# Optimization experiments

Hardware: AMD Instinct MI355X
Metric: run time of the kernel (lower is better)

Reference implementation:

```python
import jax, jax.numpy as jnp
import numpy as np

B, T, D, F, E, K = 2, 2048, 1024, 4096, 8, 2

def setup_inputs() -> dict:
    key = jax.random.key(0)
    k0, k1, k2, k3 = jax.random.split(key, 4)
    return {
        "x": jax.random.normal(k0, (B, T, D), jnp.float32),
        "Wg": jax.random.normal(k1, (D, E), jnp.float32) * (D ** -0.5),
        "W1": jax.random.normal(k2, (E, D, F), jnp.float32) * (D ** -0.5),
        "b1": jnp.zeros((E, F), jnp.float32),
        "W2": jax.random.normal(k3, (E, F, D), jnp.float32) * (F ** -0.5),
        "b2": jnp.zeros((E, D), jnp.float32),
        "topk": K,
    }

def reference(x, Wg, W1, b1, W2, b2, topk):
    n_experts = Wg.shape[-1]
    # Gating logits [B, T, E]
    gating = jnp.einsum('btd,de->bte', x, Wg)
    _, idx = jax.lax.top_k(gating, topk)
    # 0/1 mask of selected experts per token [B, T, E]
    mask = jax.nn.one_hot(idx, n_experts, dtype=x.dtype).sum(axis=-2)
    # Source does `gating -= 1/mask - 1`: no-op where mask==1, -inf where mask==0
    gate = jax.nn.softmax(jnp.where(mask > 0, gating, -jnp.inf), axis=-1)
    # Dense masked per-expert compute, exactly as the source (expert(x * mask_e))
    xm = x[:, :, None, :] * mask[:, :, :, None]          # [B, T, E, D]
    h = jax.nn.gelu(jnp.einsum('bted,edf->btef', xm, W1) + b1)  # [B, T, E, F]
    out_e = jnp.einsum('btef,efd->bted', h, W2) + b2     # [B, T, E, D]
    # Gate and sum over experts
    return jnp.sum(out_e * gate[..., None], axis=-2)      # [B, T, D]
```

## Files before the change

### kernel.cpp

```cpp
#include <hip/hip_runtime.h>
#include <hip/hip_bf16.h>
#include <math.h>

#define NB 2
#define NT 2048
#define NTOK 4096
#define DD 1024
#define FF 4096
#define NE 8
#define KSEL 2
#define BM 128
#define BN 128
#define BK 64
#define ROWCAP 9216
#define ROWTILES 72
#define KP2 2

typedef __attribute__((ext_vector_type(8))) short short8_t;
typedef __attribute__((ext_vector_type(4))) float f32x4;

__device__ __forceinline__ unsigned short f2bf(float f){
  unsigned u = __float_as_uint(f);
  unsigned r = (u + 0x7fffu + ((u >> 16) & 1u)) >> 16;
  return (unsigned short)r;
}

__device__ __forceinline__ int xcd_swz(int lin, int nwg){
  int q = nwg >> 3, r = nwg & 7;
  int xcd = lin & 7, idx = lin >> 3;
  return (xcd < r ? xcd * (q + 1) : r * (q + 1) + (xcd - r) * q) + idx;
}

#define GLOAD_LDS(g, l) \
  __builtin_amdgcn_global_load_lds((const __attribute__((address_space(1))) void*)(g), \
                                   (__attribute__((address_space(3))) void*)(l), 16, 0, 0)


__global__ void k_convert_x(const float* __restrict__ x, short* __restrict__ xb){
  int i = blockIdx.x * 256 + threadIdx.x;
  float4 v = ((const float4*)x)[i];
  short4 o;
  o.x = (short)f2bf(v.x); o.y = (short)f2bf(v.y);
  o.z = (short)f2bf(v.z); o.w = (short)f2bf(v.w);
  ((short4*)xb)[i] = o;
}

__global__ void k_transpose_convert(const float* __restrict__ in, short* __restrict__ out,
                                    int R, int C){
  __shared__ short T[64][132];
  int e = blockIdx.z;
  const float* ine = in + (size_t)e * R * C;
  short* oute = out + (size_t)e * R * C;
  int c0 = blockIdx.x * 64, r0 = blockIdx.y * 128;
  int t = threadIdx.x;
  int rr = t >> 4, c4 = (t & 15) * 4;
#pragma unroll
  for (int p = 0; p < 8; ++p){
    int row = p * 16 + rr;
    float4 v = *(const float4*)(ine + (size_t)(r0 + row) * C + c0 + c4);
    T[c4 + 0][row] = (short)f2bf(v.x);
    T[c4 + 1][row] = (short)f2bf(v.y);
    T[c4 + 2][row] = (short)f2bf(v.z);
    T[c4 + 3][row] = (short)f2bf(v.w);
  }
  __syncthreads();
  int c8 = (t & 15) * 8;
#pragma unroll
  for (int q = 0; q < 4; ++q){
    int orow = q * 16 + rr;
    short4 lo = *(const short4*)&T[orow][c8];
    short4 hi = *(const short4*)&T[orow][c8 + 4];
    short8_t w;
    w[0] = lo.x; w[1] = lo.y; w[2] = lo.z; w[3] = lo.w;
    w[4] = hi.x; w[5] = hi.y; w[6] = hi.z; w[7] = hi.w;
    *(short8_t*)(oute + (size_t)(c0 + orow) * R + r0 + c8) = w;
  }
}


__global__ void k_gating(const float* __restrict__ x, const float* __restrict__ wg,
                         int* __restrict__ topk_idx, float* __restrict__ topk_gate,
                         int* __restrict__ counts){
  int wid = threadIdx.x >> 6, lane = threadIdx.x & 63;
  int t = blockIdx.x * 4 + wid;
  const float* xr = x + (size_t)t * DD;
  double acc[NE];
#pragma unroll
  for (int e = 0; e < NE; ++e) acc[e] = 0.0;
  for (int i = 0; i < DD / 64; ++i){
    int d = i * 64 + lane;
    double xv = (double)xr[d];
    const float* wr = wg + (size_t)d * NE;
#pragma unroll
    for (int e = 0; e < NE; ++e) acc[e] += xv * (double)wr[e];
  }
#pragma unroll
  for (int e = 0; e < NE; ++e){
#pragma unroll
    for (int s = 32; s; s >>= 1) acc[e] += __shfl_xor(acc[e], s, 64);
  }
  if (lane == 0){
    int i0 = 0; double v0 = acc[0];
#pragma unroll
    for (int e = 1; e < NE; ++e) if (acc[e] > v0){ v0 = acc[e]; i0 = e; }
    int i1 = -1; double v1 = -1e300;
#pragma unroll
    for (int e = 0; e < NE; ++e) if (e != i0 && acc[e] > v1){ v1 = acc[e]; i1 = e; }
    double g0 = 1.0 / (1.0 + exp(v1 - v0));
    double g1 = 1.0 - g0;
    topk_idx[2 * t] = i0; topk_idx[2 * t + 1] = i1;
    topk_gate[2 * t] = (float)g0; topk_gate[2 * t + 1] = (float)g1;
    atomicAdd(&counts[i0], 1);
    atomicAdd(&counts[i1], 1);
  }
}

__global__ void k_scan(const int* __restrict__ counts, int* __restrict__ poff,
                       int* __restrict__ cursors, int* __restrict__ rend){
  if (threadIdx.x == 0){
    int off = 0;
    for (int e = 0; e < NE; ++e){
      poff[e] = off; cursors[e] = off; rend[e] = off + counts[e];
      off += (counts[e] + BM - 1) & ~(BM - 1);
    }
    poff[NE] = off;
  }
}

__global__ void k_route(const int* __restrict__ topk_idx, const float* __restrict__ topk_gate,
                        int* __restrict__ cursors, int* __restrict__ row_token,
                        float* __restrict__ row_gate){
  int t = blockIdx.x * 256 + threadIdx.x;
  if (t >= NTOK) return;
#pragma unroll
  for (int k = 0; k < KSEL; ++k){
    int e = topk_idx[2 * t + k];
    float g = topk_gate[2 * t + k];
    int slot = atomicAdd(&cursors[e], 1);
    row_token[slot] = t;
    row_gate[slot] = g;
  }
}


__launch_bounds__(256, 2)
__global__ void k_gemm1(const short* __restrict__ xb, const short* __restrict__ w1t,
                        const float* __restrict__ b1, short* __restrict__ h,
                        const int* __restrict__ row_token, const int* __restrict__ poff){
  __shared__ short As[BM * BK];
  __shared__ short Bs[BN * BK];
  int lin = blockIdx.x + ROWTILES * blockIdx.y;
  int wg = xcd_swz(lin, ROWTILES * (FF / BN));
  int bx = wg % ROWTILES, by = wg / ROWTILES;
  int row0 = bx * BM;
  if (row0 >= poff[NE]) return;
  int e = 0;
  while (row0 >= poff[e + 1]) ++e;
  int n0 = by * BN;
  int tid = threadIdx.x;

  const short* asrc[4]; const short* bsrc[4];
#pragma unroll
  for (int p = 0; p < 4; ++p){
    int L = p * 256 + tid;
    int r = L >> 3, cs = L & 7;
    int cd = cs ^ (r & 7);
    int tok = row_token[row0 + r];
    asrc[p] = xb + (size_t)tok * DD + cd * 8;
    bsrc[p] = w1t + (size_t)e * FF * DD + (size_t)(n0 + r) * DD + cd * 8;
  }
  short* alds = As + tid * 8;
  short* blds = Bs + tid * 8;

  f32x4 acc[4][4];
#pragma unroll
  for (int i = 0; i < 4; ++i)
#pragma unroll
    for (int j = 0; j < 4; ++j) acc[i][j] = (f32x4){0.f, 0.f, 0.f, 0.f};

  int wid = tid >> 6, lane = tid & 63;
  int wr = wid >> 1, wc = wid & 1;
  int lrow = lane & 15, lk = lane >> 4;

  for (int k0 = 0; k0 < DD; k0 += BK){
#pragma unroll
    for (int p = 0; p < 4; ++p){
      GLOAD_LDS(asrc[p] + k0, alds + p * 2048);
      GLOAD_LDS(bsrc[p] + k0, blds + p * 2048);
    }
    __syncthreads();
#pragma unroll
    for (int kk = 0; kk < 2; ++kk){
      short8_t a[4], b[4];
      int c = kk * 4 + lk;
#pragma unroll
      for (int m = 0; m < 4; ++m){
        int r = wr * 64 + m * 16 + lrow;
        a[m] = *(const short8_t*)(As + r * BK + ((c ^ (r & 7)) * 8));
      }
#pragma unroll
      for (int n = 0; n < 4; ++n){
        int r = wc * 64 + n * 16 + lrow;
        b[n] = *(const short8_t*)(Bs + r * BK + ((c ^ (r & 7)) * 8));
      }
#pragma unroll
      for (int m = 0; m < 4; ++m)
#pragma unroll
        for (int n = 0; n < 4; ++n)
          acc[m][n] = __builtin_amdgcn_mfma_f32_16x16x32_bf16(a[m], b[n], acc[m][n], 0, 0, 0);
    }
    __syncthreads();
  }

  const float* b1e = b1 + (size_t)e * FF;
#pragma unroll
  for (int n = 0; n < 4; ++n){
    int col = n0 + wc * 64 + n * 16 + lrow;
    float bias = b1e[col];
#pragma unroll
    for (int m = 0; m < 4; ++m){
#pragma unroll
      for (int j = 0; j < 4; ++j){
        int row = row0 + wr * 64 + m * 16 + lk * 4 + j;
        float v = acc[m][n][j] + bias;
        float u = 0.7978845608028654f * (v + 0.044715f * v * v * v);
        float g = v / (1.0f + __expf(-2.0f * u));
        h[(size_t)row * FF + col] = (short)f2bf(g);
      }
    }
  }
}


__launch_bounds__(256, 2)
__global__ void k_gemm2(const short* __restrict__ h, const short* __restrict__ w2t,
                        const float* __restrict__ b2, float* __restrict__ out,
                        const int* __restrict__ row_token, const float* __restrict__ row_gate,
                        const int* __restrict__ poff, const int* __restrict__ rend){
  __shared__ short As[BM * BK];
  __shared__ short Bs[BN * BK];
  int lin = blockIdx.x + ROWTILES * (blockIdx.y + (DD / BN) * blockIdx.z);
  int wg = xcd_swz(lin, ROWTILES * (DD / BN) * KP2);
  int bx = wg % ROWTILES, by = (wg / ROWTILES) % (DD / BN), kz = wg / (ROWTILES * (DD / BN));
  int row0 = bx * BM;
  if (row0 >= poff[NE]) return;
  int e = 0;
  while (row0 >= poff[e + 1]) ++e;
  int n0 = by * BN;
  int tid = threadIdx.x;

  const short* asrc[4]; const short* bsrc[4];
#pragma unroll
  for (int p = 0; p < 4; ++p){
    int L = p * 256 + tid;
    int r = L >> 3, cs = L & 7;
    int cd = cs ^ (r & 7);
    asrc[p] = h + (size_t)(row0 + r) * FF + cd * 8;
    bsrc[p] = w2t + (size_t)e * DD * FF + (size_t)(n0 + r) * FF + cd * 8;
  }
  short* alds = As + tid * 8;
  short* blds = Bs + tid * 8;

  f32x4 acc[4][4];
#pragma unroll
  for (int i = 0; i < 4; ++i)
#pragma unroll
    for (int j = 0; j < 4; ++j) acc[i][j] = (f32x4){0.f, 0.f, 0.f, 0.f};

  int wid = tid >> 6, lane = tid & 63;
  int wr = wid >> 1, wc = wid & 1;
  int lrow = lane & 15, lk = lane >> 4;

  int kbeg = kz * (FF / KP2), kend = kbeg + FF / KP2;
  for (int k0 = kbeg; k0 < kend; k0 += BK){
#pragma unroll
    for (int p = 0; p < 4; ++p){
      GLOAD_LDS(asrc[p] + k0, alds + p * 2048);
      GLOAD_LDS(bsrc[p] + k0, blds + p * 2048);
    }
    __syncthreads();
#pragma unroll
    for (int kk = 0; kk < 2; ++kk){
      short8_t a[4], b[4];
      int c = kk * 4 + lk;
#pragma unroll
      for (int m = 0; m < 4; ++m){
        int r = wr * 64 + m * 16 + lrow;
        a[m] = *(const short8_t*)(As + r * BK + ((c ^ (r & 7)) * 8));
      }
#pragma unroll
      for (int n = 0; n < 4; ++n){
        int r = wc * 64 + n * 16 + lrow;
        b[n] = *(const short8_t*)(Bs + r * BK + ((c ^ (r & 7)) * 8));
      }
#pragma unroll
      for (int m = 0; m < 4; ++m)
#pragma unroll
        for (int n = 0; n < 4; ++n)
          acc[m][n] = __builtin_amdgcn_mfma_f32_16x16x32_bf16(a[m], b[n], acc[m][n], 0, 0, 0);
    }
    __syncthreads();
  }

  int rende = rend[e];
  const float* b2e = b2 + (size_t)e * DD;
#pragma unroll
  for (int n = 0; n < 4; ++n){
    int col = n0 + wc * 64 + n * 16 + lrow;
    float bias = (kz == 0) ? b2e[col] : 0.0f;
#pragma unroll
    for (int m = 0; m < 4; ++m){
#pragma unroll
      for (int j = 0; j < 4; ++j){
        int row = row0 + wr * 64 + m * 16 + lk * 4 + j;
        if (row < rende){
          float v = acc[m][n][j] + bias;
          int tok = row_token[row];
          float g = row_gate[row];
          atomicAdd(&out[(size_t)tok * DD + col], g * v);
        }
      }
    }
  }
}


extern "C" void kernel_launch(void* const* d_in, const int* in_sizes, int n_in,
                              void* d_out, int out_size, void* d_ws, size_t ws_size,
                              hipStream_t stream){
  (void)in_sizes; (void)n_in; (void)out_size; (void)ws_size;
  const float* x  = (const float*)d_in[0];
  const float* Wg = (const float*)d_in[1];
  const float* W1 = (const float*)d_in[2];
  const float* b1 = (const float*)d_in[3];
  const float* W2 = (const float*)d_in[4];
  const float* b2 = (const float*)d_in[5];
  float* out = (float*)d_out;
  char* ws = (char*)d_ws;

  int*   counts    = (int*)(ws + 0);
  int*   poff      = (int*)(ws + 256);
  int*   cursors   = (int*)(ws + 512);
  int*   rend      = (int*)(ws + 768);
  int*   topk_idx  = (int*)(ws + 1024);
  float* topk_gate = (float*)(ws + 33792);
  int*   row_token = (int*)(ws + 66560);
  float* row_gate  = (float*)(ws + 103424);
  short* xb        = (short*)(ws + 140288);
  short* w1t       = (short*)(ws + 8528896);
  short* w2t       = (short*)(ws + 75637760);
  short* h         = (short*)(ws + 142746624);

  hipMemsetAsync(counts, 0, 32, stream);
  hipMemsetAsync(row_token, 0, ROWCAP * sizeof(int), stream);
  hipMemsetAsync(out, 0, (size_t)NTOK * DD * sizeof(float), stream);

  k_convert_x<<<dim3(NTOK * DD / 4 / 256), 256, 0, stream>>>(x, xb);
  k_transpose_convert<<<dim3(FF / 64, DD / 128, NE), 256, 0, stream>>>(W1, w1t, DD, FF);
  k_transpose_convert<<<dim3(DD / 64, FF / 128, NE), 256, 0, stream>>>(W2, w2t, FF, DD);

  k_gating<<<dim3(NTOK / 4), 256, 0, stream>>>(x, Wg, topk_idx, topk_gate, counts);
  k_scan<<<dim3(1), 64, 0, stream>>>(counts, poff, cursors, rend);
  k_route<<<dim3(NTOK / 256), 256, 0, stream>>>(topk_idx, topk_gate, cursors, row_token, row_gate);

  k_gemm1<<<dim3(ROWTILES, FF / BN), 256, 0, stream>>>(xb, w1t, b1, h, row_token, poff);
  k_gemm2<<<dim3(ROWTILES, DD / BN, KP2), 256, 0, stream>>>(h, w2t, b2, out, row_token, row_gate, poff, rend);
}
```

Before: 504.8 us.

## Fuse prep kernels, replace atomic scatter with per-slot stores plus combine kernel

Merges bf16 conversion of x with gating into one kernel and the two weight transposes into one launch. Scan and routing become a single one-block kernel that also records each token's slots and zeroes padding rows. gemm2 now writes per-split partial outputs to two buffers with plain stores instead of fp32 atomics into out, and a new combine kernel applies the gates and sums them. Also swaps the tile index mapping and raises launch bounds to 4 waves per SIMD. The gemm2 partial buffers overlap xb/w1t storage, which is safe only because gemm1 finishes first. The extra buffers and combine pass add memory traffic, and single-block routing serialises over all tokens.

```diff
diff --git a/kernel.cpp b/kernel.cpp
--- a/kernel.cpp
+++ b/kernel.cpp
@@ -36,28 +36,74 @@
                                    (__attribute__((address_space(3))) void*)(l), 16, 0, 0)
 
 
-__global__ void k_convert_x(const float* __restrict__ x, short* __restrict__ xb){
-  int i = blockIdx.x * 256 + threadIdx.x;
-  float4 v = ((const float4*)x)[i];
-  short4 o;
-  o.x = (short)f2bf(v.x); o.y = (short)f2bf(v.y);
-  o.z = (short)f2bf(v.z); o.w = (short)f2bf(v.w);
-  ((short4*)xb)[i] = o;
-}
-
-__global__ void k_transpose_convert(const float* __restrict__ in, short* __restrict__ out,
-                                    int R, int C){
+__global__ void k_prep(const float* __restrict__ x, const float* __restrict__ wg,
+                       short* __restrict__ xb, int* __restrict__ topk_idx,
+                       float* __restrict__ topk_gate, int* __restrict__ counts){
+  int wid = threadIdx.x >> 6, lane = threadIdx.x & 63;
+  int t = blockIdx.x * 4 + wid;
+  const float* xr = x + (size_t)t * DD;
+  short* xbr = xb + (size_t)t * DD;
+  double acc[NE];
+#pragma unroll
+  for (int e = 0; e < NE; ++e) acc[e] = 0.0;
+#pragma unroll
+  for (int p = 0; p < 4; ++p){
+    int d = p * 256 + lane * 4;
+    float4 v = *(const float4*)(xr + d);
+    short4 o;
+    o.x = (short)f2bf(v.x); o.y = (short)f2bf(v.y);
+    o.z = (short)f2bf(v.z); o.w = (short)f2bf(v.w);
+    *(short4*)(xbr + d) = o;
+    const float* w0 = wg + (size_t)d * NE;
+    float vv[4] = {v.x, v.y, v.z, v.w};
+#pragma unroll
+    for (int j = 0; j < 4; ++j){
+      double xv = (double)vv[j];
+#pragma unroll
+      for (int e = 0; e < NE; ++e) acc[e] += xv * (double)w0[j * NE + e];
+    }
+  }
+#pragma unroll
+  for (int e = 0; e < NE; ++e){
+#pragma unroll
+    for (int s = 32; s; s >>= 1) acc[e] += __shfl_xor(acc[e], s, 64);
+  }
+  if (lane == 0){
+    int i0 = 0; double v0 = acc[0];
+#pragma unroll
+    for (int e = 1; e < NE; ++e) if (acc[e] > v0){ v0 = acc[e]; i0 = e; }
+    int i1 = -1; double v1 = -1e300;
+#pragma unroll
+    for (int e = 0; e < NE; ++e) if (e != i0 && acc[e] > v1){ v1 = acc[e]; i1 = e; }
+    double g0 = 1.0 / (1.0 + exp(v1 - v0));
+    topk_idx[2 * t] = i0; topk_idx[2 * t + 1] = i1;
+    topk_gate[2 * t] = (float)g0; topk_gate[2 * t + 1] = (float)(1.0 - g0);
+    atomicAdd(&counts[i0], 1);
+    atomicAdd(&counts[i1], 1);
+  }
+}
+
+
+__global__ void k_transpose_all(const float* __restrict__ W1, const float* __restrict__ W2,
+                                short* __restrict__ w1t, short* __restrict__ w2t){
   __shared__ short T[64][132];
-  int e = blockIdx.z;
-  const float* ine = in + (size_t)e * R * C;
-  short* oute = out + (size_t)e * R * C;
-  int c0 = blockIdx.x * 64, r0 = blockIdx.y * 128;
+  int id = blockIdx.x;
+  bool isW2 = id >= 4096;
+  int rem = id & 4095;
+  int e = rem >> 9;
+  int tr = rem & 511;
+  int R, C, c0, r0;
+  const float* in; short* out;
+  if (!isW2){ R = DD; C = FF; c0 = (tr & 63) * 64; r0 = (tr >> 6) * 128;
+              in = W1 + (size_t)e * R * C; out = w1t + (size_t)e * R * C; }
+  else      { R = FF; C = DD; c0 = (tr & 15) * 64; r0 = (tr >> 4) * 128;
+              in = W2 + (size_t)e * R * C; out = w2t + (size_t)e * R * C; }
   int t = threadIdx.x;
   int rr = t >> 4, c4 = (t & 15) * 4;
 #pragma unroll
   for (int p = 0; p < 8; ++p){
     int row = p * 16 + rr;
-    float4 v = *(const float4*)(ine + (size_t)(r0 + row) * C + c0 + c4);
+    float4 v = *(const float4*)(in + (size_t)(r0 + row) * C + c0 + c4);
     T[c4 + 0][row] = (short)f2bf(v.x);
     T[c4 + 1][row] = (short)f2bf(v.y);
     T[c4 + 2][row] = (short)f2bf(v.z);
@@ -73,77 +119,47 @@
     short8_t w;
     w[0] = lo.x; w[1] = lo.y; w[2] = lo.z; w[3] = lo.w;
     w[4] = hi.x; w[5] = hi.y; w[6] = hi.z; w[7] = hi.w;
-    *(short8_t*)(oute + (size_t)(c0 + orow) * R + r0 + c8) = w;
-  }
-}
-
-
-__global__ void k_gating(const float* __restrict__ x, const float* __restrict__ wg,
-                         int* __restrict__ topk_idx, float* __restrict__ topk_gate,
-                         int* __restrict__ counts){
-  int wid = threadIdx.x >> 6, lane = threadIdx.x & 63;
-  int t = blockIdx.x * 4 + wid;
-  const float* xr = x + (size_t)t * DD;
-  double acc[NE];
-#pragma unroll
-  for (int e = 0; e < NE; ++e) acc[e] = 0.0;
-  for (int i = 0; i < DD / 64; ++i){
-    int d = i * 64 + lane;
-    double xv = (double)xr[d];
-    const float* wr = wg + (size_t)d * NE;
-#pragma unroll
-    for (int e = 0; e < NE; ++e) acc[e] += xv * (double)wr[e];
-  }
-#pragma unroll
-  for (int e = 0; e < NE; ++e){
-#pragma unroll
-    for (int s = 32; s; s >>= 1) acc[e] += __shfl_xor(acc[e], s, 64);
-  }
-  if (lane == 0){
-    int i0 = 0; double v0 = acc[0];
-#pragma unroll
-    for (int e = 1; e < NE; ++e) if (acc[e] > v0){ v0 = acc[e]; i0 = e; }
-    int i1 = -1; double v1 = -1e300;
-#pragma unroll
-    for (int e = 0; e < NE; ++e) if (e != i0 && acc[e] > v1){ v1 = acc[e]; i1 = e; }
-    double g0 = 1.0 / (1.0 + exp(v1 - v0));
-    double g1 = 1.0 - g0;
-    topk_idx[2 * t] = i0; topk_idx[2 * t + 1] = i1;
-    topk_gate[2 * t] = (float)g0; topk_gate[2 * t + 1] = (float)g1;
-    atomicAdd(&counts[i0], 1);
-    atomicAdd(&counts[i1], 1);
-  }
-}
-
-__global__ void k_scan(const int* __restrict__ counts, int* __restrict__ poff,
-                       int* __restrict__ cursors, int* __restrict__ rend){
+    *(short8_t*)(out + (size_t)(c0 + orow) * R + r0 + c8) = w;
+  }
+}
+
+
+__global__ void k_route_all(const int* __restrict__ counts, const int* __restrict__ topk_idx,
+                            const float* __restrict__ topk_gate, int* __restrict__ poff_g,
+                            int* __restrict__ row_token, float* __restrict__ row_gate,
+                            int* __restrict__ slot_of){
+  __shared__ int poff[NE + 1], cur[NE], rends[NE];
   if (threadIdx.x == 0){
     int off = 0;
     for (int e = 0; e < NE; ++e){
-      poff[e] = off; cursors[e] = off; rend[e] = off + counts[e];
+      poff[e] = off; cur[e] = off; rends[e] = off + counts[e];
       off += (counts[e] + BM - 1) & ~(BM - 1);
     }
     poff[NE] = off;
-  }
-}
-
-__global__ void k_route(const int* __restrict__ topk_idx, const float* __restrict__ topk_gate,
-                        int* __restrict__ cursors, int* __restrict__ row_token,
-                        float* __restrict__ row_gate){
-  int t = blockIdx.x * 256 + threadIdx.x;
-  if (t >= NTOK) return;
-#pragma unroll
-  for (int k = 0; k < KSEL; ++k){
-    int e = topk_idx[2 * t + k];
-    float g = topk_gate[2 * t + k];
-    int slot = atomicAdd(&cursors[e], 1);
-    row_token[slot] = t;
-    row_gate[slot] = g;
-  }
-}
-
-
-__launch_bounds__(256, 2)
+    for (int e = 0; e <= NE; ++e) poff_g[e] = poff[e];
+  }
+  __syncthreads();
+  for (int t = threadIdx.x; t < NTOK; t += 256){
+#pragma unroll
+    for (int k = 0; k < KSEL; ++k){
+      int e = topk_idx[2 * t + k];
+      float g = topk_gate[2 * t + k];
+      int slot = atomicAdd(&cur[e], 1);
+      row_token[slot] = t;
+      row_gate[slot] = g;
+      slot_of[2 * t + k] = slot;
+    }
+  }
+  __syncthreads();
+#pragma unroll
+  for (int e = 0; e < NE; ++e)
+    for (int s = rends[e] + (int)threadIdx.x; s < poff[e + 1]; s += 256){
+      row_token[s] = 0; row_gate[s] = 0.f;
+    }
+}
+
+
+__launch_bounds__(256, 4)
 __global__ void k_gemm1(const short* __restrict__ xb, const short* __restrict__ w1t,
                         const float* __restrict__ b1, short* __restrict__ h,
                         const int* __restrict__ row_token, const int* __restrict__ poff){
@@ -151,7 +167,7 @@
   __shared__ short Bs[BN * BK];
   int lin = blockIdx.x + ROWTILES * blockIdx.y;
   int wg = xcd_swz(lin, ROWTILES * (FF / BN));
-  int bx = wg % ROWTILES, by = wg / ROWTILES;
+  int bx = wg >> 5, by = wg & 31;
   int row0 = bx * BM;
   if (row0 >= poff[NE]) return;
   int e = 0;
@@ -232,16 +248,15 @@
 }
 
 
-__launch_bounds__(256, 2)
+__launch_bounds__(256, 4)
 __global__ void k_gemm2(const short* __restrict__ h, const short* __restrict__ w2t,
-                        const float* __restrict__ b2, float* __restrict__ out,
-                        const int* __restrict__ row_token, const float* __restrict__ row_gate,
-                        const int* __restrict__ poff, const int* __restrict__ rend){
+                        const float* __restrict__ b2, float* __restrict__ ya,
+                        float* __restrict__ yb, const int* __restrict__ poff){
   __shared__ short As[BM * BK];
   __shared__ short Bs[BN * BK];
   int lin = blockIdx.x + ROWTILES * (blockIdx.y + (DD / BN) * blockIdx.z);
   int wg = xcd_swz(lin, ROWTILES * (DD / BN) * KP2);
-  int bx = wg % ROWTILES, by = (wg / ROWTILES) % (DD / BN), kz = wg / (ROWTILES * (DD / BN));
+  int by = wg & 7, bx = (wg >> 3) % ROWTILES, kz = (wg >> 3) / ROWTILES;
   int row0 = bx * BM;
   if (row0 >= poff[NE]) return;
   int e = 0;
@@ -302,7 +317,7 @@
     __syncthreads();
   }
 
-  int rende = rend[e];
+  float* y = (kz == 0) ? ya : yb;
   const float* b2e = b2 + (size_t)e * DD;
 #pragma unroll
   for (int n = 0; n < 4; ++n){
@@ -313,15 +328,31 @@
 #pragma unroll
       for (int j = 0; j < 4; ++j){
         int row = row0 + wr * 64 + m * 16 + lk * 4 + j;
-        if (row < rende){
-          float v = acc[m][n][j] + bias;
-          int tok = row_token[row];
-          float g = row_gate[row];
-          atomicAdd(&out[(size_t)tok * DD + col], g * v);
-        }
-      }
-    }
-  }
+        y[(size_t)row * DD + col] = acc[m][n][j] + bias;
+      }
+    }
+  }
+}
+
+
+__global__ void k_combine(const float* __restrict__ ya, const float* __restrict__ yb,
+                          const int* __restrict__ slot_of, const float* __restrict__ topk_gate,
+                          float* __restrict__ out){
+  int i = blockIdx.x * 256 + threadIdx.x;
+  int t = i >> 8;
+  int c4 = (i & 255) * 4;
+  int s0 = slot_of[2 * t], s1 = slot_of[2 * t + 1];
+  float g0 = topk_gate[2 * t], g1 = topk_gate[2 * t + 1];
+  float4 a0 = *(const float4*)(ya + (size_t)s0 * DD + c4);
+  float4 b0 = *(const float4*)(yb + (size_t)s0 * DD + c4);
+  float4 a1 = *(const float4*)(ya + (size_t)s1 * DD + c4);
+  float4 b1 = *(const float4*)(yb + (size_t)s1 * DD + c4);
+  float4 o;
+  o.x = g0 * (a0.x + b0.x) + g1 * (a1.x + b1.x);
+  o.y = g0 * (a0.y + b0.y) + g1 * (a1.y + b1.y);
+  o.z = g0 * (a0.z + b0.z) + g1 * (a1.z + b1.z);
+  o.w = g0 * (a0.w + b0.w) + g1 * (a1.w + b1.w);
+  *(float4*)(out + (size_t)t * DD + c4) = o;
 }
 
 
@@ -340,29 +371,25 @@
 
   int*   counts    = (int*)(ws + 0);
   int*   poff      = (int*)(ws + 256);
-  int*   cursors   = (int*)(ws + 512);
-  int*   rend      = (int*)(ws + 768);
   int*   topk_idx  = (int*)(ws + 1024);
   float* topk_gate = (float*)(ws + 33792);
   int*   row_token = (int*)(ws + 66560);
   float* row_gate  = (float*)(ws + 103424);
-  short* xb        = (short*)(ws + 140288);
-  short* w1t       = (short*)(ws + 8528896);
-  short* w2t       = (short*)(ws + 75637760);
-  short* h         = (short*)(ws + 142746624);
+  int*   slot_of   = (int*)(ws + 140288);
+  short* xb        = (short*)(ws + 173056);
+  short* w1t       = (short*)(ws + 8561664);
+  short* w2t       = (short*)(ws + 75670528);
+  short* h         = (short*)(ws + 142779392);
+  float* ya        = (float*)(ws + 173056);
+  float* yb        = (float*)(ws + 37921792);
 
   hipMemsetAsync(counts, 0, 32, stream);
-  hipMemsetAsync(row_token, 0, ROWCAP * sizeof(int), stream);
-  hipMemsetAsync(out, 0, (size_t)NTOK * DD * sizeof(float), stream);
-
-  k_convert_x<<<dim3(NTOK * DD / 4 / 256), 256, 0, stream>>>(x, xb);
-  k_transpose_convert<<<dim3(FF / 64, DD / 128, NE), 256, 0, stream>>>(W1, w1t, DD, FF);
-  k_transpose_convert<<<dim3(DD / 64, FF / 128, NE), 256, 0, stream>>>(W2, w2t, FF, DD);
-
-  k_gating<<<dim3(NTOK / 4), 256, 0, stream>>>(x, Wg, topk_idx, topk_gate, counts);
-  k_scan<<<dim3(1), 64, 0, stream>>>(counts, poff, cursors, rend);
-  k_route<<<dim3(NTOK / 256), 256, 0, stream>>>(topk_idx, topk_gate, cursors, row_token, row_gate);
-
+
+  k_prep<<<dim3(NTOK / 4), 256, 0, stream>>>(x, Wg, xb, topk_idx, topk_gate, counts);
+  k_transpose_all<<<dim3(8192), 256, 0, stream>>>(W1, W2, w1t, w2t);
+  k_route_all<<<dim3(1), 256, 0, stream>>>(counts, topk_idx, topk_gate, poff,
+                                           row_token, row_gate, slot_of);
   k_gemm1<<<dim3(ROWTILES, FF / BN), 256, 0, stream>>>(xb, w1t, b1, h, row_token, poff);
-  k_gemm2<<<dim3(ROWTILES, DD / BN, KP2), 256, 0, stream>>>(h, w2t, b2, out, row_token, row_gate, poff, rend);
-}
+  k_gemm2<<<dim3(ROWTILES, DD / BN, KP2), 256, 0, stream>>>(h, w2t, b2, ya, yb, poff);
+  k_combine<<<dim3(NTOK * DD / 4 / 256), 256, 0, stream>>>(ya, yb, slot_of, topk_gate, out);
+}
```

Measured after the change: 473.9 us. -6.1%, faster.
